# Performance work log

Hardware: AMD Instinct MI355X
Metric: run time of the kernel (lower is better)

The kernel has to match this reference:

```python
import jax, jax.numpy as jnp
import numpy as np

N_SPECIES = 4
NNZ = 16384
N_CELLS = 512
N_LATENT = 256
H = 1024
N_GENES = 20000


def setup_inputs() -> dict:
    key = jax.random.key(0)
    ks = jax.random.split(key, 8)
    scale = 0.02
    return {
        "values": jax.random.normal(ks[0], (NNZ,), jnp.float32),
        "batch_idx": jax.random.randint(ks[1], (NNZ,), 0, N_CELLS, jnp.int64 if jax.config.jax_enable_x64 else jnp.int32),
        "gene_idx": jax.random.randint(ks[2], (NNZ,), 0, N_GENES, jnp.int64 if jax.config.jax_enable_x64 else jnp.int32),
        "global_latent": jax.random.normal(ks[3], (N_CELLS, N_LATENT), jnp.float32),
        "z": jax.random.normal(ks[4], (N_SPECIES, NNZ // N_SPECIES, N_LATENT), jnp.float32),
        "W1": jax.random.normal(ks[5], (N_SPECIES, 2 * N_LATENT, H), jnp.float32) * scale,
        "b1": jnp.zeros((N_SPECIES, H), jnp.float32),
        "W2": jax.random.normal(ks[6], (N_SPECIES, H, H), jnp.float32) * scale,
        "b2": jnp.zeros((N_SPECIES, H), jnp.float32),
        "W3": jax.random.normal(ks[7], (N_SPECIES, H, N_GENES), jnp.float32) * scale,
        "b3": jnp.zeros((N_SPECIES, N_GENES), jnp.float32),
    }


def reference(values, batch_idx, gene_idx, global_latent, z, W1, b1, W2, b2, W3, b3):
    # species_mask is a static equal partition of the nnz entries: species i
    # owns entries [i*m, (i+1)*m). Dropout is identity (eval mode).
    n_species, m, _ = z.shape
    out_parts = []
    for i in range(n_species):
        bi = batch_idx[i * m:(i + 1) * m]          # [m] cell indices (< m and < N_CELLS)
        gi = gene_idx[i * m:(i + 1) * m]           # [m] gene indices
        expanded_global = global_latent[bi]        # [m, L]
        combined = jnp.concatenate([z[i], expanded_global], axis=1)  # [m, 2L]
        h = jax.nn.relu(combined @ W1[i] + b1[i])  # [m, H]
        h = jax.nn.relu(h @ W2[i] + b2[i])         # [m, H]
        decoded = h @ W3[i] + b3[i]                # [m, n_genes] -- full matmul as in source
        out_parts.append(jax.nn.softplus(decoded[bi, gi]))  # gather one scalar per entry
    # output starts as zeros_like(values); every entry is written by its species.
    output = jnp.zeros_like(values)
    output = jnp.concatenate(out_parts, axis=0) + output * 0.0
    return output
```

## Files before the change

### kernel.cpp

```cpp
#include <hip/hip_runtime.h>
#include <hip/hip_bf16.h>
#include <math.h>

#define N_SPECIES 4
#define NNZ       16384
#define MPS       4096
#define N_CELLS   512
#define N_LATENT  256
#define HDIM      1024
#define N_GENES   20000

#define STRIPE    128
#define NSTRIPE   157
#define NBUCKET   (N_SPECIES * NSTRIPE)
#define CAP       128
#define KCHUNK    32
#define KSLICE    64
#define NSLICE    (HDIM / KSLICE)

typedef __bf16 bf16x8 __attribute__((ext_vector_type(8)));
typedef float  f32x4  __attribute__((ext_vector_type(4)));

static __device__ __forceinline__ unsigned short f2b(float f) {
    __hip_bfloat16 h = __float2bfloat16(f);
    return __builtin_bit_cast(unsigned short, h);
}
static __device__ __forceinline__ float b2f(unsigned short u) {
    return __builtin_bit_cast(float, (unsigned int)u << 16);
}
static __device__ __forceinline__ float softplusf(float x) {
    return (x > 20.f) ? x : log1pf(expf(x));
}

__global__ __launch_bounds__(256) void transpose_w12(
    const float* __restrict__ W1, const float* __restrict__ W2,
    unsigned short* __restrict__ Wt1, unsigned short* __restrict__ Wt2)
{
    __shared__ float tile[32][33];
    int s = blockIdx.z, y = blockIdx.y;
    const float* Ws; unsigned short* Wts; int K, k0;
    if (y < 16) { Ws = W1 + (size_t)s * 512 * HDIM;  Wts = Wt1 + (size_t)s * HDIM * 512;  K = 512;  k0 = y * 32; }
    else        { Ws = W2 + (size_t)s * HDIM * HDIM; Wts = Wt2 + (size_t)s * HDIM * HDIM; K = HDIM; k0 = (y - 16) * 32; }
    int n0 = blockIdx.x * 32;
    int tx = threadIdx.x, ty = threadIdx.y;
    #pragma unroll
    for (int p = 0; p < 4; p++)
        tile[ty + 8 * p][tx] = Ws[(size_t)(k0 + ty + 8 * p) * HDIM + n0 + tx];
    __syncthreads();
    #pragma unroll
    for (int p = 0; p < 4; p++) {
        int r = ty + 8 * p;
        Wts[(size_t)(n0 + r) * K + k0 + tx] = f2b(tile[tx][r]);
    }
}

__global__ __launch_bounds__(256) void gemm1_fused(
    const float* __restrict__ z, const float* __restrict__ gl,
    const int* __restrict__ bidx, const unsigned short* __restrict__ Bt,
    const float* __restrict__ bias, unsigned short* __restrict__ C)
{
    int s = blockIdx.z;
    const unsigned short* Bs = Bt + (size_t)s * HDIM * 512;
    const float* bvec = bias + (size_t)s * HDIM;
    int m0 = blockIdx.x * 64, n0 = blockIdx.y * 64;

    __shared__ unsigned short Alds[64 * 64];
    __shared__ unsigned short Blds[64 * 64];

    int tid = threadIdx.x, lane = tid & 63, w = tid >> 6;
    int wr = w >> 1, wc = w & 1;
    f32x4 acc[2][2] = {};

    for (int kt = 0; kt < 512; kt += 64) {
        #pragma unroll
        for (int it = 0; it < 2; it++) {
            int c = it * 256 + tid;
            int row = c >> 3, kb = c & 7;
            int pa = kb ^ (row & 7);
            int col = kt + kb * 8;
            const float* src;
            if (col < N_LATENT)
                src = z + ((size_t)s * MPS + m0 + row) * N_LATENT + col;
            else
                src = gl + (size_t)bidx[s * MPS + m0 + row] * N_LATENT + (col - N_LATENT);
            float4 f0 = *(const float4*)src;
            float4 f1 = *(const float4*)(src + 4);
            unsigned short o[8] = { f2b(f0.x), f2b(f0.y), f2b(f0.z), f2b(f0.w),
                                    f2b(f1.x), f2b(f1.y), f2b(f1.z), f2b(f1.w) };
            *(uint4*)(Alds + row * 64 + pa * 8) = *(const uint4*)o;
            uint4 vb = *(const uint4*)(Bs + (size_t)(n0 + row) * 512 + kt + kb * 8);
            *(uint4*)(Blds + row * 64 + pa * 8) = vb;
        }
        __syncthreads();
        #pragma unroll
        for (int ks = 0; ks < 2; ks++) {
            bf16x8 af[2], bfr[2];
            #pragma unroll
            for (int f = 0; f < 2; f++) {
                int ar  = wr * 32 + f * 16 + (lane & 15);
                int akb = (ks * 4 + (lane >> 4)) ^ (ar & 7);
                af[f]  = __builtin_bit_cast(bf16x8, *(const uint4*)(Alds + ar * 64 + akb * 8));
                int br  = wc * 32 + f * 16 + (lane & 15);
                int bkb = (ks * 4 + (lane >> 4)) ^ (br & 7);
                bfr[f] = __builtin_bit_cast(bf16x8, *(const uint4*)(Blds + br * 64 + bkb * 8));
            }
            #pragma unroll
            for (int fm = 0; fm < 2; fm++)
                #pragma unroll
                for (int fn = 0; fn < 2; fn++)
                    acc[fm][fn] = __builtin_amdgcn_mfma_f32_16x16x32_bf16(
                        af[fm], bfr[fn], acc[fm][fn], 0, 0, 0);
        }
        __syncthreads();
    }

    #pragma unroll
    for (int fm = 0; fm < 2; fm++)
        #pragma unroll
        for (int fn = 0; fn < 2; fn++) {
            int col = n0 + wc * 32 + fn * 16 + (lane & 15);
            float bv = bvec[col];
            #pragma unroll
            for (int r = 0; r < 4; r++) {
                int row = m0 + wr * 32 + fm * 16 + (lane >> 4) * 4 + r;
                float v = fmaxf(acc[fm][fn][r] + bv, 0.0f);
                C[(size_t)s * N_CELLS * HDIM + (size_t)row * HDIM + col] = f2b(v);
            }
        }
}

__global__ __launch_bounds__(256) void gemm_bf16_mfma(
    const unsigned short* __restrict__ A, const unsigned short* __restrict__ Bt,
    const float* __restrict__ bias, unsigned short* __restrict__ C,
    int M, int N, int K)
{
    int s = blockIdx.z;
    const unsigned short* As = A  + (size_t)s * M * K;
    const unsigned short* Bs = Bt + (size_t)s * N * K;
    const float* bvec = bias + (size_t)s * N;
    int m0 = blockIdx.x * 64, n0 = blockIdx.y * 64;

    __shared__ unsigned short Alds[64 * 64];
    __shared__ unsigned short Blds[64 * 64];

    int tid = threadIdx.x, lane = tid & 63, w = tid >> 6;
    int wr = w >> 1, wc = w & 1;
    f32x4 acc[2][2] = {};

    for (int kt = 0; kt < K; kt += 64) {
        #pragma unroll
        for (int it = 0; it < 2; it++) {
            int c = it * 256 + tid;
            int row = c >> 3, kb = c & 7;
            int pa = kb ^ (row & 7);
            uint4 va = *(const uint4*)(As + (size_t)(m0 + row) * K + kt + kb * 8);
            *(uint4*)(Alds + row * 64 + pa * 8) = va;
            uint4 vb = *(const uint4*)(Bs + (size_t)(n0 + row) * K + kt + kb * 8);
            *(uint4*)(Blds + row * 64 + pa * 8) = vb;
        }
        __syncthreads();
        #pragma unroll
        for (int ks = 0; ks < 2; ks++) {
            bf16x8 af[2], bfr[2];
            #pragma unroll
            for (int f = 0; f < 2; f++) {
                int ar  = wr * 32 + f * 16 + (lane & 15);
                int akb = (ks * 4 + (lane >> 4)) ^ (ar & 7);
                af[f]  = __builtin_bit_cast(bf16x8, *(const uint4*)(Alds + ar * 64 + akb * 8));
                int br  = wc * 32 + f * 16 + (lane & 15);
                int bkb = (ks * 4 + (lane >> 4)) ^ (br & 7);
                bfr[f] = __builtin_bit_cast(bf16x8, *(const uint4*)(Blds + br * 64 + bkb * 8));
            }
            #pragma unroll
            for (int fm = 0; fm < 2; fm++)
                #pragma unroll
                for (int fn = 0; fn < 2; fn++)
                    acc[fm][fn] = __builtin_amdgcn_mfma_f32_16x16x32_bf16(
                        af[fm], bfr[fn], acc[fm][fn], 0, 0, 0);
        }
        __syncthreads();
    }

    #pragma unroll
    for (int fm = 0; fm < 2; fm++)
        #pragma unroll
        for (int fn = 0; fn < 2; fn++) {
            int col = n0 + wc * 32 + fn * 16 + (lane & 15);
            float bv = bvec[col];
            #pragma unroll
            for (int r = 0; r < 4; r++) {
                int row = m0 + wr * 32 + fm * 16 + (lane >> 4) * 4 + r;
                float v = fmaxf(acc[fm][fn][r] + bv, 0.0f);
                C[(size_t)s * M * N + (size_t)row * N + col] = f2b(v);
            }
        }
}

__global__ __launch_bounds__(256) void zero_aux(
    int* __restrict__ counts, float* __restrict__ partial, int4* __restrict__ lists4)
{
    int i = blockIdx.x * 256 + threadIdx.x;
    if (i <= NBUCKET) counts[i] = 0;
    if (i < NSLICE * NNZ) partial[i] = 0.f;
    if (i < NBUCKET * CAP) lists4[i] = make_int4(0, 0, 0, 0);
}

__global__ __launch_bounds__(256) void bucket_pack(
    const int* __restrict__ bidx, const int* __restrict__ gidx,
    int* __restrict__ counts, int4* __restrict__ lists4, int* __restrict__ ovf_list)
{
    int j = blockIdx.x * 256 + threadIdx.x;
    int s = j >> 12;
    int g = gidx[j];
    int sb = s * NSTRIPE + (g >> 7);
    int pos = atomicAdd(&counts[sb], 1);
    if (pos < CAP) lists4[sb * CAP + pos] = make_int4(j, bidx[j], g, 0);
    else           ovf_list[atomicAdd(&counts[NBUCKET], 1)] = j;
}

__global__ __launch_bounds__(256) void decode_slice(
    const unsigned short* __restrict__ H2b, const int* __restrict__ bidx,
    const int* __restrict__ gidx, const float* __restrict__ W3,
    const int* __restrict__ counts, const int4* __restrict__ lists4,
    const int* __restrict__ ovf_list, float* __restrict__ partial)
{
    __shared__ float tile[STRIPE][KCHUNK + 1];
    int sb = blockIdx.x, sl = blockIdx.y;
    int s  = sb / NSTRIPE;
    int g0 = (sb % NSTRIPE) * STRIPE;
    int tid = threadIdx.x, lane = tid & 63, w = tid >> 6;
    int hw = lane >> 5, l32 = lane & 31;
    int k0 = sl * KSLICE;
    const float* Ws = W3 + (size_t)s * HDIM * N_GENES;

    int rb = tid >> 5;
    int gq = tid & 31;
    int gcl = g0 + gq * 4;
    gcl = (gcl <= N_GENES - 4) ? gcl : (N_GENES - 4);
    float4 q[8];
    #pragma unroll
    for (int c = 0; c < 2; c++)
        #pragma unroll
        for (int p = 0; p < 4; p++)
            q[c * 4 + p] = *(const float4*)(
                Ws + (size_t)(k0 + c * 32 + p * 8 + rb) * N_GENES + gcl);

    int cnt = counts[sb];
    int jj[8], gg[8];
    float hv[8][2];
    {
        int4 L[8];
        #pragma unroll
        for (int e = 0; e < 8; e++)
            L[e] = lists4[sb * CAP + (e * 8 + w * 2 + hw)];
        #pragma unroll
        for (int e = 0; e < 8; e++) {
            const unsigned short* hp = H2b + ((size_t)s * N_CELLS + L[e].y) * HDIM + k0;
            hv[e][0] = b2f(hp[l32]);
            hv[e][1] = b2f(hp[32 + l32]);
            jj[e] = L[e].x;
            gg[e] = L[e].z & (STRIPE - 1);
        }
    }

    float acc[8] = {};
    #pragma unroll
    for (int p = 0; p < 4; p++)
        #pragma unroll
        for (int u = 0; u < 4; u++)
            tile[gq * 4 + u][p * 8 + rb] = ((const float*)&q[p])[u];
    __syncthreads();
    #pragma unroll
    for (int e = 0; e < 8; e++)
        acc[e] += hv[e][0] * tile[gg[e]][l32];
    __syncthreads();
    #pragma unroll
    for (int p = 0; p < 4; p++)
        #pragma unroll
        for (int u = 0; u < 4; u++)
            tile[gq * 4 + u][p * 8 + rb] = ((const float*)&q[4 + p])[u];
    __syncthreads();
    #pragma unroll
    for (int e = 0; e < 8; e++)
        acc[e] += hv[e][1] * tile[gg[e]][l32];

    #pragma unroll
    for (int e = 0; e < 8; e++) {
        float sum = acc[e];
        sum += __shfl_xor(sum, 16, 64);
        sum += __shfl_xor(sum,  8, 64);
        sum += __shfl_xor(sum,  4, 64);
        sum += __shfl_xor(sum,  2, 64);
        sum += __shfl_xor(sum,  1, 64);
        int li = e * 8 + w * 2 + hw;
        if (li < cnt && l32 == 0)
            partial[(size_t)sl * NNZ + jj[e]] = sum;
    }

    for (int base = 64; base < cnt; base += 64) {
        int jj2[8], gg2[8];
        float hv2[8][2];
        #pragma unroll
        for (int e = 0; e < 8; e++) {
            int li = base + e * 8 + w * 2 + hw;
            if (li < cnt) {
                int4 Le = lists4[sb * CAP + li];
                jj2[e] = Le.x;
                const unsigned short* hp = H2b + ((size_t)s * N_CELLS + Le.y) * HDIM + k0;
                hv2[e][0] = b2f(hp[l32]);
                hv2[e][1] = b2f(hp[32 + l32]);
                gg2[e] = Le.z & (STRIPE - 1);
            } else { jj2[e] = -1; hv2[e][0] = hv2[e][1] = 0.f; gg2[e] = 0; }
        }
        float a2[8] = {};
        #pragma unroll
        for (int c = 0; c < 2; c++) {
            __syncthreads();
            #pragma unroll
            for (int p = 0; p < 4; p++) {
                float4 v = *(const float4*)(
                    Ws + (size_t)(k0 + c * 32 + p * 8 + rb) * N_GENES + gcl);
                #pragma unroll
                for (int u = 0; u < 4; u++)
                    tile[gq * 4 + u][p * 8 + rb] = ((const float*)&v)[u];
            }
            __syncthreads();
            #pragma unroll
            for (int e = 0; e < 8; e++)
                a2[e] += hv2[e][c] * tile[gg2[e]][l32];
        }
        #pragma unroll
        for (int e = 0; e < 8; e++) {
            float sum = a2[e];
            sum += __shfl_xor(sum, 16, 64);
            sum += __shfl_xor(sum,  8, 64);
            sum += __shfl_xor(sum,  4, 64);
            sum += __shfl_xor(sum,  2, 64);
            sum += __shfl_xor(sum,  1, 64);
            if (jj2[e] >= 0 && l32 == 0)
                partial[(size_t)sl * NNZ + jj2[e]] = sum;
        }
    }

    if (sl == 0) {
        int novf = counts[NBUCKET];
        for (int i = sb * 4 + w; i < novf; i += NBUCKET * 4) {
            int j = ovf_list[i];
            int es = j >> 12;
            int bi = bidx[j], gi = gidx[j];
            const unsigned short* h = H2b + ((size_t)es * N_CELLS + bi) * HDIM;
            const float* wcol = W3 + (size_t)es * HDIM * N_GENES + gi;
            float sum = 0.f;
            #pragma unroll
            for (int t = 0; t < HDIM / 64; t++) {
                int k = t * 64 + lane;
                sum += b2f(h[k]) * wcol[(size_t)k * N_GENES];
            }
            #pragma unroll
            for (int off = 32; off; off >>= 1)
                sum += __shfl_xor(sum, off, 64);
            if (lane == 0) partial[j] = sum;
        }
    }
}

__global__ __launch_bounds__(256) void finalize_out(
    const float* __restrict__ partial, const int* __restrict__ gidx,
    const float* __restrict__ b3, float* __restrict__ out)
{
    int j = blockIdx.x * 256 + threadIdx.x;
    int s = j >> 12;
    float x = b3[(size_t)s * N_GENES + gidx[j]];
    #pragma unroll
    for (int sl = 0; sl < NSLICE; sl++)
        x += partial[(size_t)sl * NNZ + j];
    out[j] = softplusf(x);
}

extern "C" void kernel_launch(void* const* d_in, const int* in_sizes, int n_in,
                              void* d_out, int out_size, void* d_ws, size_t ws_size,
                              hipStream_t stream) {
    const int*   batch_idx = (const int*)  d_in[1];
    const int*   gene_idx  = (const int*)  d_in[2];
    const float* gl        = (const float*)d_in[3];
    const float* z         = (const float*)d_in[4];
    const float* W1        = (const float*)d_in[5];
    const float* b1        = (const float*)d_in[6];
    const float* W2        = (const float*)d_in[7];
    const float* b2        = (const float*)d_in[8];
    const float* W3        = (const float*)d_in[9];
    const float* b3        = (const float*)d_in[10];
    float* out = (float*)d_out;

    char* ws = (char*)d_ws;
    unsigned short* Wt1   = (unsigned short*)(ws + 0);
    unsigned short* Wt2   = (unsigned short*)(ws + (4ull  << 20));
    unsigned short* H1    = (unsigned short*)(ws + (12ull << 20));
    unsigned short* H2b   = (unsigned short*)(ws + (16ull << 20));
    int*            counts   = (int*)       (ws + (20ull << 20));
    int4*           lists4   = (int4*)      (ws + (21ull << 20));
    int*            ovf_list = (int*)       (ws + (23ull << 20));
    float*          partial  = (float*)     (ws + (24ull << 20));

    zero_aux<<<(NBUCKET * CAP + 255) / 256, 256, 0, stream>>>(counts, partial, lists4);
    bucket_pack<<<NNZ / 256, 256, 0, stream>>>(batch_idx, gene_idx, counts, lists4, ovf_list);

    transpose_w12<<<dim3(HDIM / 32, 48, N_SPECIES), dim3(32, 8), 0, stream>>>(W1, W2, Wt1, Wt2);

    gemm1_fused<<<dim3(N_CELLS / 64, HDIM / 64, N_SPECIES), 256, 0, stream>>>(
        z, gl, batch_idx, Wt1, b1, H1);

    gemm_bf16_mfma<<<dim3(N_CELLS / 64, HDIM / 64, N_SPECIES), 256, 0, stream>>>(
        H1, Wt2, b2, H2b, N_CELLS, HDIM, HDIM);

    decode_slice<<<dim3(NBUCKET, NSLICE), 256, 0, stream>>>(
        H2b, batch_idx, gene_idx, W3, counts, lists4, ovf_list, partial);

    finalize_out<<<NNZ / 256, 256, 0, stream>>>(partial, gene_idx, b3, out);
}
```

Measured before the change: 115.7 us.

## Fuse W1/W2 transpose-convert into GEMM B staging and shrink zeroing kernel

Removes the separate transpose_w12 kernel. GEMM1 and GEMM2 now read the fp32 W1/W2 directly, converting them to bf16 and transposing while staging B into LDS. The aux zeroing kernel now clears only the bucket counts. Overflow entries zero their other partial slices inline, and bucket list row indices are masked so stale list entries stay in bounds. This saves a launch and a full weight-rewrite pass, but each GEMM tile re-reads fp32 weights (twice the bytes) and uses scalar 2-byte scattered LDS stores, which can cause bank conflicts.

```diff
diff --git a/kernel.cpp b/kernel.cpp
--- a/kernel.cpp
+++ b/kernel.cpp
@@ -32,35 +32,32 @@
     return (x > 20.f) ? x : log1pf(expf(x));
 }
 
-__global__ __launch_bounds__(256) void transpose_w12(
-    const float* __restrict__ W1, const float* __restrict__ W2,
-    unsigned short* __restrict__ Wt1, unsigned short* __restrict__ Wt2)
-{
-    __shared__ float tile[32][33];
-    int s = blockIdx.z, y = blockIdx.y;
-    const float* Ws; unsigned short* Wts; int K, k0;
-    if (y < 16) { Ws = W1 + (size_t)s * 512 * HDIM;  Wts = Wt1 + (size_t)s * HDIM * 512;  K = 512;  k0 = y * 32; }
-    else        { Ws = W2 + (size_t)s * HDIM * HDIM; Wts = Wt2 + (size_t)s * HDIM * HDIM; K = HDIM; k0 = (y - 16) * 32; }
-    int n0 = blockIdx.x * 32;
-    int tx = threadIdx.x, ty = threadIdx.y;
-    #pragma unroll
-    for (int p = 0; p < 4; p++)
-        tile[ty + 8 * p][tx] = Ws[(size_t)(k0 + ty + 8 * p) * HDIM + n0 + tx];
-    __syncthreads();
+static __device__ __forceinline__ void stage_B_f32(
+    const float* __restrict__ W, int ldw, int kt, int n0, int tid,
+    unsigned short* __restrict__ Blds)
+{
     #pragma unroll
     for (int p = 0; p < 4; p++) {
-        int r = ty + 8 * p;
-        Wts[(size_t)(n0 + r) * K + k0 + tx] = f2b(tile[tx][r]);
+        int idx = p * 256 + tid;
+        int kr = idx >> 4;
+        int nc = (idx & 15) * 4;
+        float4 v = *(const float4*)(W + (size_t)(kt + kr) * ldw + n0 + nc);
+        int blk = kr >> 3, kin = kr & 7;
+        #pragma unroll
+        for (int u = 0; u < 4; u++) {
+            int n = nc + u;
+            Blds[n * 64 + ((blk ^ (n & 7)) << 3) + kin] = f2b(((const float*)&v)[u]);
+        }
     }
 }
 
 __global__ __launch_bounds__(256) void gemm1_fused(
     const float* __restrict__ z, const float* __restrict__ gl,
-    const int* __restrict__ bidx, const unsigned short* __restrict__ Bt,
+    const int* __restrict__ bidx, const float* __restrict__ W1,
     const float* __restrict__ bias, unsigned short* __restrict__ C)
 {
     int s = blockIdx.z;
-    const unsigned short* Bs = Bt + (size_t)s * HDIM * 512;
+    const float* Bs = W1 + (size_t)s * 512 * HDIM;
     const float* bvec = bias + (size_t)s * HDIM;
     int m0 = blockIdx.x * 64, n0 = blockIdx.y * 64;
 
@@ -88,9 +85,8 @@
             unsigned short o[8] = { f2b(f0.x), f2b(f0.y), f2b(f0.z), f2b(f0.w),
                                     f2b(f1.x), f2b(f1.y), f2b(f1.z), f2b(f1.w) };
             *(uint4*)(Alds + row * 64 + pa * 8) = *(const uint4*)o;
-            uint4 vb = *(const uint4*)(Bs + (size_t)(n0 + row) * 512 + kt + kb * 8);
-            *(uint4*)(Blds + row * 64 + pa * 8) = vb;
-        }
+        }
+        stage_B_f32(Bs, HDIM, kt, n0, tid, Blds);
         __syncthreads();
         #pragma unroll
         for (int ks = 0; ks < 2; ks++) {
@@ -129,15 +125,14 @@
         }
 }
 
-__global__ __launch_bounds__(256) void gemm_bf16_mfma(
-    const unsigned short* __restrict__ A, const unsigned short* __restrict__ Bt,
-    const float* __restrict__ bias, unsigned short* __restrict__ C,
-    int M, int N, int K)
+__global__ __launch_bounds__(256) void gemm2_fused(
+    const unsigned short* __restrict__ A, const float* __restrict__ W2,
+    const float* __restrict__ bias, unsigned short* __restrict__ C)
 {
     int s = blockIdx.z;
-    const unsigned short* As = A  + (size_t)s * M * K;
-    const unsigned short* Bs = Bt + (size_t)s * N * K;
-    const float* bvec = bias + (size_t)s * N;
+    const unsigned short* As = A + (size_t)s * N_CELLS * HDIM;
+    const float* Bs = W2 + (size_t)s * HDIM * HDIM;
+    const float* bvec = bias + (size_t)s * HDIM;
     int m0 = blockIdx.x * 64, n0 = blockIdx.y * 64;
 
     __shared__ unsigned short Alds[64 * 64];
@@ -147,17 +142,16 @@
     int wr = w >> 1, wc = w & 1;
     f32x4 acc[2][2] = {};
 
-    for (int kt = 0; kt < K; kt += 64) {
+    for (int kt = 0; kt < HDIM; kt += 64) {
         #pragma unroll
         for (int it = 0; it < 2; it++) {
             int c = it * 256 + tid;
             int row = c >> 3, kb = c & 7;
             int pa = kb ^ (row & 7);
-            uint4 va = *(const uint4*)(As + (size_t)(m0 + row) * K + kt + kb * 8);
+            uint4 va = *(const uint4*)(As + (size_t)(m0 + row) * HDIM + kt + kb * 8);
             *(uint4*)(Alds + row * 64 + pa * 8) = va;
-            uint4 vb = *(const uint4*)(Bs + (size_t)(n0 + row) * K + kt + kb * 8);
-            *(uint4*)(Blds + row * 64 + pa * 8) = vb;
-        }
+        }
+        stage_B_f32(Bs, HDIM, kt, n0, tid, Blds);
         __syncthreads();
         #pragma unroll
         for (int ks = 0; ks < 2; ks++) {
@@ -191,18 +185,15 @@
             for (int r = 0; r < 4; r++) {
                 int row = m0 + wr * 32 + fm * 16 + (lane >> 4) * 4 + r;
                 float v = fmaxf(acc[fm][fn][r] + bv, 0.0f);
-                C[(size_t)s * M * N + (size_t)row * N + col] = f2b(v);
-            }
-        }
-}
-
-__global__ __launch_bounds__(256) void zero_aux(
-    int* __restrict__ counts, float* __restrict__ partial, int4* __restrict__ lists4)
+                C[(size_t)s * N_CELLS * HDIM + (size_t)row * HDIM + col] = f2b(v);
+            }
+        }
+}
+
+__global__ __launch_bounds__(256) void zero_counts(int* __restrict__ counts)
 {
     int i = blockIdx.x * 256 + threadIdx.x;
     if (i <= NBUCKET) counts[i] = 0;
-    if (i < NSLICE * NNZ) partial[i] = 0.f;
-    if (i < NBUCKET * CAP) lists4[i] = make_int4(0, 0, 0, 0);
 }
 
 __global__ __launch_bounds__(256) void bucket_pack(
@@ -255,7 +246,8 @@
             L[e] = lists4[sb * CAP + (e * 8 + w * 2 + hw)];
         #pragma unroll
         for (int e = 0; e < 8; e++) {
-            const unsigned short* hp = H2b + ((size_t)s * N_CELLS + L[e].y) * HDIM + k0;
+            const unsigned short* hp =
+                H2b + ((size_t)s * N_CELLS + (L[e].y & (N_CELLS - 1))) * HDIM + k0;
             hv[e][0] = b2f(hp[l32]);
             hv[e][1] = b2f(hp[32 + l32]);
             jj[e] = L[e].x;
@@ -359,7 +351,12 @@
             #pragma unroll
             for (int off = 32; off; off >>= 1)
                 sum += __shfl_xor(sum, off, 64);
-            if (lane == 0) partial[j] = sum;
+            if (lane == 0) {
+                partial[j] = sum;
+                #pragma unroll
+                for (int z2 = 1; z2 < NSLICE; z2++)
+                    partial[(size_t)z2 * NNZ + j] = 0.f;
+            }
         }
     }
 }
@@ -393,25 +390,21 @@
     float* out = (float*)d_out;
 
     char* ws = (char*)d_ws;
-    unsigned short* Wt1   = (unsigned short*)(ws + 0);
-    unsigned short* Wt2   = (unsigned short*)(ws + (4ull  << 20));
-    unsigned short* H1    = (unsigned short*)(ws + (12ull << 20));
-    unsigned short* H2b   = (unsigned short*)(ws + (16ull << 20));
-    int*            counts   = (int*)       (ws + (20ull << 20));
-    int4*           lists4   = (int4*)      (ws + (21ull << 20));
-    int*            ovf_list = (int*)       (ws + (23ull << 20));
-    float*          partial  = (float*)     (ws + (24ull << 20));
-
-    zero_aux<<<(NBUCKET * CAP + 255) / 256, 256, 0, stream>>>(counts, partial, lists4);
+    unsigned short* H1    = (unsigned short*)(ws + 0);
+    unsigned short* H2b   = (unsigned short*)(ws + (4ull  << 20));
+    int*            counts   = (int*)       (ws + (8ull  << 20));
+    int4*           lists4   = (int4*)      (ws + (9ull  << 20));
+    int*            ovf_list = (int*)       (ws + (11ull << 20));
+    float*          partial  = (float*)     (ws + (12ull << 20));
+
+    zero_counts<<<(NBUCKET + 256) / 256, 256, 0, stream>>>(counts);
     bucket_pack<<<NNZ / 256, 256, 0, stream>>>(batch_idx, gene_idx, counts, lists4, ovf_list);
 
-    transpose_w12<<<dim3(HDIM / 32, 48, N_SPECIES), dim3(32, 8), 0, stream>>>(W1, W2, Wt1, Wt2);
-
     gemm1_fused<<<dim3(N_CELLS / 64, HDIM / 64, N_SPECIES), 256, 0, stream>>>(
-        z, gl, batch_idx, Wt1, b1, H1);
-
-    gemm_bf16_mfma<<<dim3(N_CELLS / 64, HDIM / 64, N_SPECIES), 256, 0, stream>>>(
-        H1, Wt2, b2, H2b, N_CELLS, HDIM, HDIM);
+        z, gl, batch_idx, W1, b1, H1);
+
+    gemm2_fused<<<dim3(N_CELLS / 64, HDIM / 64, N_SPECIES), 256, 0, stream>>>(
+        H1, W2, b2, H2b);
 
     decode_slice<<<dim3(NBUCKET, NSLICE), 256, 0, stream>>>(
         H2b, batch_idx, gene_idx, W3, counts, lists4, ovf_list, partial);
```

New measurement: 136.2 us. 1.18x slower.
